# Optimization experiments

Hardware: AMD Instinct MI355X
Metric: run time of the kernel (lower is better)

## Reference

```python
import jax, jax.numpy as jnp
import numpy as np
from jax import lax

N, D, H, E = 8192, 1024, 4096, 8


def setup_inputs() -> dict:
    key = jax.random.key(0)
    ks = jax.random.split(key, 4)
    return {
        "x": jax.random.normal(ks[0], (N, D), dtype=jnp.float32),
        "wg": jax.random.normal(ks[1], (D, E), dtype=jnp.float32) * 0.001,
        "fc1_w": jax.random.normal(ks[2], (E, D, H), dtype=jnp.float32) * 0.001,
        "fc1_b": jnp.zeros((E, 1, H), dtype=jnp.float32),
        "fc2_w": jax.random.normal(ks[3], (E, H, D), dtype=jnp.float32) * 0.001,
        "fc2_b": jnp.zeros((E, 1, D), dtype=jnp.float32),
        "k": 2,
    }


def reference(x, wg, fc1_w, fc1_b, fc2_w, fc2_b, k):
    n, d = x.shape
    e = wg.shape[1]
    cap = (k * n) // e  # expert capacity (capacity factor 1.0)

    # --- gate ---
    scores = jax.nn.softmax(x @ wg, axis=-1)          # [N,E]
    topv, topi = lax.top_k(scores, k)                 # [N,k]

    # --- top-k routing: position of each (token, slot) within its expert buffer ---
    masks = jax.nn.one_hot(topi, e, dtype=jnp.int32)  # [N,k,E]
    # slot-major priority: all slot-0 assignments before slot-1
    m = jnp.transpose(masks, (1, 0, 2)).reshape(k * n, e)
    pos_flat = jnp.cumsum(m, axis=0) - m              # position before own assignment
    pos = jnp.sum(pos_flat * m, axis=1).reshape(k, n).T   # [N,k]
    valid = pos < cap                                  # capacity overflow -> dropped

    # --- load-balance aux loss (top-1 fraction * mean gate prob) ---
    me = scores.mean(axis=0)                           # [E]
    ce = masks[:, 0, :].astype(scores.dtype).mean(axis=0)
    l_aux = e * jnp.sum(me * ce)

    # --- encode (dispatch): scatter tokens into [E, C, D] buffers ---
    w = valid.astype(x.dtype)                          # [N,k]
    flat_idx = topi * cap + jnp.where(valid, pos, 0)   # [N,k]
    contrib = (x[:, None, :] * w[:, :, None]).reshape(-1, d)
    dispatched = jnp.zeros((e * cap, d), x.dtype).at[flat_idx.reshape(-1)].add(contrib)
    dispatched = dispatched.reshape(e, cap, d)

    # --- batched expert FFN (all-to-all is identity on one device) ---
    h = jax.nn.relu(jnp.einsum('ecd,edh->ech', dispatched, fc1_w) + fc1_b)
    y = jnp.einsum('ech,ehd->ecd', h, fc2_w) + fc2_b   # [E,C,D]

    # --- decode (combine): gather back and weight by gate scores ---
    gathered = y.reshape(e * cap, d)[flat_idx]         # [N,k,D]
    output = jnp.einsum('nk,nkd->nd', topv * w, gathered)
    return output, l_aux
```

## Files before the change

### kernel.cpp

```cpp
#include <hip/hip_runtime.h>
#include <hip/hip_bf16.h>
#include <stdint.h>

#define N_TOK 8192
#define DMODEL 1024
#define HDIM 4096
#define NEXP 8
#define CAP 2048
#define GATE_BLOCKS (N_TOK / 4)

typedef float floatx4 __attribute__((ext_vector_type(4)));
typedef int int32x4_t __attribute__((ext_vector_type(4)));
typedef int int32x8_t __attribute__((ext_vector_type(8)));

static __device__ __forceinline__ void async_copy16(const void* g, void* l) {
  __builtin_amdgcn_global_load_lds(
      (const __attribute__((address_space(1))) void*)g,
      (__attribute__((address_space(3))) void*)l, 16, 0, 0);
}

static __device__ __forceinline__ unsigned int pk4_fp8(float a, float b, float c, float d) {
  int r = __builtin_amdgcn_cvt_pk_fp8_f32(a, b, 0, 0);
  r = __builtin_amdgcn_cvt_pk_fp8_f32(c, d, r, 1);
  return (unsigned int)r;
}

static __device__ __forceinline__ unsigned short f2bf(float f) {
  union { float f; uint32_t u; } v; v.f = f;
  uint32_t r = (v.u + 0x7FFFu + ((v.u >> 16) & 1u)) >> 16;
  return (unsigned short)r;
}

static __device__ __forceinline__ float bf2f(unsigned short u) {
  union { float f; uint32_t u32; } v; v.u32 = ((uint32_t)u) << 16;
  return v.f;
}

__global__ __launch_bounds__(256) void gate_kernel(
    const float* __restrict__ x, const float* __restrict__ wg,
    float* __restrict__ topv, int* __restrict__ topi,
    float* __restrict__ me_part, int* __restrict__ ce_part) {
  __shared__ float sm_p[4][NEXP];
  __shared__ int sm_i0[4];
  int wave = threadIdx.x >> 6;
  int lane = threadIdx.x & 63;
  int n = blockIdx.x * 4 + wave;
  float acc[NEXP];
#pragma unroll
  for (int e = 0; e < NEXP; e++) acc[e] = 0.f;
  const float* xr = x + (size_t)n * DMODEL;
#pragma unroll 4
  for (int i = 0; i < DMODEL / 64; i++) {
    int idx = lane + 64 * i;
    float xv = xr[idx];
    const float4* wr = (const float4*)(wg + (size_t)idx * NEXP);
    float4 w0 = wr[0], w1 = wr[1];
    acc[0] += xv * w0.x; acc[1] += xv * w0.y;
    acc[2] += xv * w0.z; acc[3] += xv * w0.w;
    acc[4] += xv * w1.x; acc[5] += xv * w1.y;
    acc[6] += xv * w1.z; acc[7] += xv * w1.w;
  }
#pragma unroll
  for (int e = 0; e < NEXP; e++) {
    float v = acc[e];
#pragma unroll
    for (int off = 32; off > 0; off >>= 1) v += __shfl_down(v, off, 64);
    acc[e] = v;
  }
  if (lane == 0) {
    float mx = acc[0];
#pragma unroll
    for (int e = 1; e < NEXP; e++) mx = fmaxf(mx, acc[e]);
    float p[NEXP]; float s = 0.f;
#pragma unroll
    for (int e = 0; e < NEXP; e++) { p[e] = expf(acc[e] - mx); s += p[e]; }
    float inv = 1.f / s;
#pragma unroll
    for (int e = 0; e < NEXP; e++) p[e] *= inv;
    int i0 = 0; float v0 = p[0];
#pragma unroll
    for (int e = 1; e < NEXP; e++) if (p[e] > v0) { v0 = p[e]; i0 = e; }
    int i1 = -1; float v1 = -1.f;
#pragma unroll
    for (int e = 0; e < NEXP; e++) {
      if (e == i0) continue;
      if (p[e] > v1) { v1 = p[e]; i1 = e; }
    }
    topv[n * 2] = v0; topv[n * 2 + 1] = v1;
    topi[n * 2] = i0; topi[n * 2 + 1] = i1;
#pragma unroll
    for (int e = 0; e < NEXP; e++) sm_p[wave][e] = p[e];
    sm_i0[wave] = i0;
  }
  __syncthreads();
  if (threadIdx.x < NEXP) {
    int e = threadIdx.x;
    float pm = 0.f; int cc = 0;
#pragma unroll
    for (int w = 0; w < 4; w++) {
      pm += sm_p[w][e];
      cc += (sm_i0[w] == e) ? 1 : 0;
    }
    me_part[blockIdx.x * NEXP + e] = pm;
    ce_part[blockIdx.x * NEXP + e] = cc;
  }
}

__global__ __launch_bounds__(1024) void scan_kernel(
    const int* __restrict__ topi, const float* __restrict__ topv,
    int* __restrict__ flat_idx, float* __restrict__ cw) {
  __shared__ int hist[16][NEXP];
  __shared__ int base[NEXP];
  int tid = threadIdx.x;
  int w = tid >> 6, lane = tid & 63;
  if (tid < NEXP) base[tid] = 0;
  int vals[16];
#pragma unroll
  for (int c = 0; c < 16; c++) {
    int j = c * 1024 + tid;
    vals[c] = topi[(size_t)(j & 8191) * 2 + (j >> 13)];
  }
  __syncthreads();
  for (int c = 0; c < 16; c++) {
    int j = c * 1024 + tid;
    int slot = j >> 13;
    int n = j & 8191;
    int e = vals[c];
    int rank = 0;
#pragma unroll
    for (int ee = 0; ee < NEXP; ee++) {
      unsigned long long m = __ballot(e == ee);
      if (e == ee) rank = __popcll(m & ((1ull << lane) - 1ull));
      if (lane == ee) hist[w][ee] = __popcll(m);
    }
    __syncthreads();
    if (tid < NEXP) {
      int run = base[tid];
#pragma unroll
      for (int ww = 0; ww < 16; ww++) {
        int t = hist[ww][tid];
        hist[ww][tid] = run;
        run += t;
      }
      base[tid] = run;
    }
    __syncthreads();
    int pos = hist[w][e] + rank;
    bool valid = pos < CAP;
    flat_idx[n * 2 + slot] = e * CAP + (valid ? pos : 0);
    cw[n * 2 + slot] = valid ? topv[n * 2 + slot] : 0.f;
    __syncthreads();
  }
}

__global__ __launch_bounds__(256) void transpose_cvt_fp8(
    const float* __restrict__ in, unsigned char* __restrict__ out,
    int R, int C) {
  __shared__ float tile[32][129];
  const float* inp = in + (size_t)blockIdx.z * R * C;
  unsigned char* outp = out + (size_t)blockIdx.z * R * C;
  int c0 = blockIdx.x * 32, r0 = blockIdx.y * 128;
  int t = threadIdx.x;
#pragma unroll
  for (int p = 0; p < 4; p++) {
    int r = p * 32 + (t >> 3);
    int c4 = (t & 7) * 4;
    float4 v = *(const float4*)(inp + (size_t)(r0 + r) * C + c0 + c4);
    tile[c4 + 0][r] = v.x; tile[c4 + 1][r] = v.y;
    tile[c4 + 2][r] = v.z; tile[c4 + 3][r] = v.w;
  }
  __syncthreads();
  int c = t >> 3, r16 = (t & 7) * 16;
  unsigned int w[4];
#pragma unroll
  for (int j = 0; j < 4; j++) {
    float a = tile[c][r16 + j * 4 + 0] * 512.f;
    float b = tile[c][r16 + j * 4 + 1] * 512.f;
    float cc2 = tile[c][r16 + j * 4 + 2] * 512.f;
    float d = tile[c][r16 + j * 4 + 3] * 512.f;
    w[j] = pk4_fp8(a, b, cc2, d);
  }
  uint4 o; o.x = w[0]; o.y = w[1]; o.z = w[2]; o.w = w[3];
  *(uint4*)(outp + (size_t)(c0 + c) * R + r0 + r16) = o;
}

__global__ __launch_bounds__(64) void dispatch_kernel(
    const float* __restrict__ x, const int* __restrict__ flat_idx,
    const float* __restrict__ cw, unsigned char* __restrict__ disp) {
  int a = blockIdx.x;
  if (cw[a] == 0.f) return;
  int n = a >> 1;
  int f = flat_idx[a];
  int lane = threadIdx.x;
  const float4* xr = (const float4*)(x + (size_t)n * DMODEL);
  unsigned int* dr = (unsigned int*)(disp + (size_t)f * DMODEL);
#pragma unroll
  for (int i = 0; i < 4; i++) {
    float4 v = xr[lane + 64 * i];
    dr[lane + 64 * i] = pk4_fp8(v.x, v.y, v.z, v.w);
  }
}

template <int K_DIM, bool RELU, int OUT_MODE>
__global__ __launch_bounds__(512) void gemm_fp8_kernel(
    const unsigned char* __restrict__ A, const unsigned char* __restrict__ BT,
    const float* __restrict__ bias, void* __restrict__ Cout, int M, int Ncols,
    float inv_scale, float out_mult) {
  constexpr int BK = 128;
  constexpr int NSTAGE = K_DIM / BK;
  static_assert(NSTAGE >= 2, "need >=2 K stages for the 2-deep pipeline");
  __shared__ unsigned char As[2][256 * BK];
  __shared__ unsigned char Bs[2][256 * BK];

  int e = blockIdx.z, tm = blockIdx.y, tn = blockIdx.x;
  const unsigned char* Ae = A + (size_t)e * M * K_DIM + (size_t)tm * 256 * K_DIM;
  const unsigned char* Be = BT + (size_t)e * Ncols * K_DIM + (size_t)tn * 256 * K_DIM;
  int wv = threadIdx.x >> 6, l = threadIdx.x & 63;
  int wm = wv >> 2, wn = wv & 3;
  int l15 = l & 15, quad = l >> 4;
  int rbase = wv * 8 + (l >> 3);
  int cg = (l & 7) ^ ((l >> 3) & 7);
  floatx4 acc[8][4] = {};

#define STAGE_LOADS(k0, buf)                                                   \
  {                                                                            \
    _Pragma("unroll") for (int i = 0; i < 4; i++) {                            \
      int r = rbase + i * 64;                                                  \
      async_copy16(Ae + (size_t)r * K_DIM + (k0) + cg * 16,                    \
                   &As[buf][i * 8192 + wv * 1024]);                            \
      async_copy16(Be + (size_t)r * K_DIM + (k0) + cg * 16,                    \
                   &Bs[buf][i * 8192 + wv * 1024]);                            \
    }                                                                          \
  }

#define READ_BF(ni)                                                            \
  {                                                                            \
    int m = wn * 64 + (ni) * 16 + l15;                                         \
    int x0 = (quad * 2) ^ (m & 7), x1 = (quad * 2 + 1) ^ (m & 7);              \
    int32x4_t lo = *(const int32x4_t*)(&Bs[cur][m * 128 + x0 * 16]);           \
    int32x4_t hi = *(const int32x4_t*)(&Bs[cur][m * 128 + x1 * 16]);           \
    bf[ni] = __builtin_shufflevector(lo, hi, 0, 1, 2, 3, 4, 5, 6, 7);          \
  }

#define READ_AF(dst, mi)                                                       \
  {                                                                            \
    int m = wm * 128 + (mi) * 16 + l15;                                        \
    int x0 = (quad * 2) ^ (m & 7), x1 = (quad * 2 + 1) ^ (m & 7);              \
    int32x4_t lo = *(const int32x4_t*)(&As[cur][m * 128 + x0 * 16]);           \
    int32x4_t hi = *(const int32x4_t*)(&As[cur][m * 128 + x1 * 16]);           \
    (dst) = __builtin_shufflevector(lo, hi, 0, 1, 2, 3, 4, 5, 6, 7);           \
  }

#define MFMA_ROW(asrc, mi)                                                     \
  _Pragma("unroll") for (int ni = 0; ni < 4; ni++)                             \
      acc[mi][ni] = __builtin_amdgcn_mfma_scale_f32_16x16x128_f8f6f4(          \
          (asrc), bf[ni], acc[mi][ni], 0, 0, 0, 0x7F7F7F7F, 0, 0x7F7F7F7F);

  STAGE_LOADS(0, 0);
  STAGE_LOADS(BK, 1);
#pragma unroll
  for (int s = 0; s < NSTAGE; s++) {
    const int cur = s & 1;
    if (s + 1 < NSTAGE)
      asm volatile("s_waitcnt vmcnt(8)" ::: "memory");
    else
      asm volatile("s_waitcnt vmcnt(0)" ::: "memory");
    __builtin_amdgcn_s_barrier();
    int32x8_t afA[4], afB[4], bf[4];
    READ_BF(0); READ_BF(1); READ_BF(2); READ_BF(3);
    READ_AF(afA[0], 0);
    __builtin_amdgcn_sched_barrier(0);
    READ_AF(afA[1], 1);
    __builtin_amdgcn_sched_barrier(0);
    READ_AF(afA[2], 2);
    __builtin_amdgcn_sched_barrier(0);
    READ_AF(afA[3], 3);
    __builtin_amdgcn_sched_barrier(0);
    __builtin_amdgcn_s_setprio(1);
    asm volatile("s_waitcnt lgkmcnt(6)" ::: "memory");
    __builtin_amdgcn_sched_barrier(0);
    MFMA_ROW(afA[0], 0);
    asm volatile("s_waitcnt lgkmcnt(4)" ::: "memory");
    __builtin_amdgcn_sched_barrier(0);
    MFMA_ROW(afA[1], 1);
    asm volatile("s_waitcnt lgkmcnt(2)" ::: "memory");
    __builtin_amdgcn_sched_barrier(0);
    MFMA_ROW(afA[2], 2);
    asm volatile("s_waitcnt lgkmcnt(0)" ::: "memory");
    __builtin_amdgcn_sched_barrier(0);
    MFMA_ROW(afA[3], 3);
    __builtin_amdgcn_s_setprio(0);
    READ_AF(afB[0], 4);
    __builtin_amdgcn_sched_barrier(0);
    READ_AF(afB[1], 5);
    __builtin_amdgcn_sched_barrier(0);
    READ_AF(afB[2], 6);
    __builtin_amdgcn_sched_barrier(0);
    READ_AF(afB[3], 7);
    __builtin_amdgcn_sched_barrier(0);
    __builtin_amdgcn_s_setprio(1);
    asm volatile("s_waitcnt lgkmcnt(6)" ::: "memory");
    __builtin_amdgcn_sched_barrier(0);
    MFMA_ROW(afB[0], 4);
    asm volatile("s_waitcnt lgkmcnt(4)" ::: "memory");
    __builtin_amdgcn_sched_barrier(0);
    MFMA_ROW(afB[1], 5);
    asm volatile("s_waitcnt lgkmcnt(2)" ::: "memory");
    __builtin_amdgcn_sched_barrier(0);
    MFMA_ROW(afB[2], 6);
    asm volatile("s_waitcnt lgkmcnt(0)" ::: "memory");
    __builtin_amdgcn_sched_barrier(0);
    __builtin_amdgcn_s_setprio(0);
    __builtin_amdgcn_s_barrier();
    if (s + 2 < NSTAGE) STAGE_LOADS((s + 2) * BK, cur);
    __builtin_amdgcn_s_setprio(1);
    MFMA_ROW(afB[3], 7);
    __builtin_amdgcn_s_setprio(0);
  }
#undef STAGE_LOADS
#undef READ_BF
#undef READ_AF
#undef MFMA_ROW

  int row_base = tm * 256 + wm * 128;
  int col_base = tn * 256 + wn * 64;
  const float* be = bias + (size_t)e * Ncols;
#pragma unroll
  for (int ni = 0; ni < 4; ni++) {
    int col = col_base + ni * 16 + l15;
    float bv = be[col];
#pragma unroll
    for (int mi = 0; mi < 8; mi++) {
#pragma unroll
      for (int r = 0; r < 4; r++) {
        int row = row_base + mi * 16 + quad * 4 + r;
        float v = acc[mi][ni][r] * inv_scale + bv;
        if (RELU) v = fmaxf(v, 0.f);
        size_t idx = (size_t)e * M * Ncols + (size_t)row * Ncols + col;
        if (OUT_MODE == 1) {
          float s = fminf(fmaxf(v * out_mult, -440.f), 440.f);
          unsigned int b8 = (unsigned int)__builtin_amdgcn_cvt_pk_fp8_f32(s, s, 0, 0) & 0xFF;
          ((unsigned char*)Cout)[idx] = (unsigned char)b8;
        } else if (OUT_MODE == 2) {
          ((unsigned short*)Cout)[idx] = f2bf(v);
        } else {
          ((float*)Cout)[idx] = v;
        }
      }
    }
  }
}

__global__ __launch_bounds__(256) void combine_kernel(
    const unsigned short* __restrict__ y, const int* __restrict__ flat_idx,
    const float* __restrict__ cw, float* __restrict__ out) {
  int n = blockIdx.x;
  float w0 = cw[n * 2], w1 = cw[n * 2 + 1];
  int f0 = flat_idx[n * 2], f1 = flat_idx[n * 2 + 1];
  const ushort2* y0 = (const ushort2*)(y + (size_t)f0 * DMODEL);
  const ushort2* y1 = (const ushort2*)(y + (size_t)f1 * DMODEL);
  float2* o = (float2*)(out + (size_t)n * DMODEL);
  int t = threadIdx.x;
#pragma unroll
  for (int i = 0; i < 2; i++) {
    int j = t + i * 256;
    ushort2 a = y0[j], b = y1[j];
    float2 r;
    r.x = w0 * bf2f(a.x) + w1 * bf2f(b.x);
    r.y = w0 * bf2f(a.y) + w1 * bf2f(b.y);
    o[j] = r;
  }
}

__global__ __launch_bounds__(256) void laux_kernel(
    const float* __restrict__ me_part, const int* __restrict__ ce_part,
    float* __restrict__ out_laux) {
  __shared__ float sme[NEXP][33];
  __shared__ float sce[NEXP][33];
  int tid = threadIdx.x;
  int e = tid >> 5;
  int c = tid & 31;
  float pm = 0.f, cc = 0.f;
  for (int b = c; b < GATE_BLOCKS; b += 32) {
    pm += me_part[b * NEXP + e];
    cc += (float)ce_part[b * NEXP + e];
  }
  sme[e][c] = pm;
  sce[e][c] = cc;
  __syncthreads();
  if (tid < NEXP) {
    float tm = 0.f, tc = 0.f;
#pragma unroll
    for (int i = 0; i < 32; i++) { tm += sme[tid][i]; tc += sce[tid][i]; }
    sme[tid][32] = tm;
    sce[tid][32] = tc;
  }
  __syncthreads();
  if (tid == 0) {
    float s = 0.f;
#pragma unroll
    for (int ee = 0; ee < NEXP; ee++)
      s += (sme[ee][32] / (float)N_TOK) * (sce[ee][32] / (float)N_TOK);
    *out_laux = (float)NEXP * s;
  }
}

extern "C" void kernel_launch(void* const* d_in, const int* in_sizes, int n_in,
                              void* d_out, int out_size, void* d_ws,
                              size_t ws_size, hipStream_t stream) {
  (void)in_sizes; (void)n_in; (void)out_size; (void)ws_size;
  const float* x     = (const float*)d_in[0];
  const float* wg    = (const float*)d_in[1];
  const float* fc1_w = (const float*)d_in[2];
  const float* fc1_b = (const float*)d_in[3];
  const float* fc2_w = (const float*)d_in[4];
  const float* fc2_b = (const float*)d_in[5];
  float* out = (float*)d_out;

  char* ws = (char*)d_ws;
  size_t o = 0;
  unsigned char* fc1t = (unsigned char*)(ws + o); o += (size_t)NEXP * DMODEL * HDIM;
  unsigned char* fc2t = (unsigned char*)(ws + o); o += (size_t)NEXP * DMODEL * HDIM;
  unsigned char* disp = (unsigned char*)(ws + o); o += (size_t)NEXP * CAP * DMODEL;
  unsigned char* hbuf = (unsigned char*)(ws + o); o += (size_t)NEXP * CAP * HDIM;
  unsigned short* ybuf = (unsigned short*)(ws + o); o += (size_t)NEXP * CAP * DMODEL * 2;
  float* topv = (float*)(ws + o); o += (size_t)N_TOK * 2 * 4;
  int* topi   = (int*)(ws + o);   o += (size_t)N_TOK * 2 * 4;
  int* flat   = (int*)(ws + o);   o += (size_t)N_TOK * 2 * 4;
  float* cw   = (float*)(ws + o); o += (size_t)N_TOK * 2 * 4;
  float* mep  = (float*)(ws + o); o += (size_t)GATE_BLOCKS * NEXP * 4;
  int* cep    = (int*)(ws + o);   o += (size_t)GATE_BLOCKS * NEXP * 4;


  gate_kernel<<<GATE_BLOCKS, 256, 0, stream>>>(x, wg, topv, topi, mep, cep);
  scan_kernel<<<1, 1024, 0, stream>>>(topi, topv, flat, cw);
  transpose_cvt_fp8<<<dim3(HDIM / 32, DMODEL / 128, NEXP), 256, 0, stream>>>(fc1_w, fc1t, DMODEL, HDIM);
  transpose_cvt_fp8<<<dim3(DMODEL / 32, HDIM / 128, NEXP), 256, 0, stream>>>(fc2_w, fc2t, HDIM, DMODEL);
  dispatch_kernel<<<N_TOK * 2, 64, 0, stream>>>(x, flat, cw, disp);
  gemm_fp8_kernel<DMODEL, true, 1>
      <<<dim3(HDIM / 256, CAP / 256, NEXP), 512, 0, stream>>>(
          disp, fc1t, fc1_b, hbuf, CAP, HDIM, 1.f / 512.f, 16.f);
  gemm_fp8_kernel<HDIM, false, 2>
      <<<dim3(DMODEL / 256, CAP / 256, NEXP), 512, 0, stream>>>(
          hbuf, fc2t, fc2_b, ybuf, CAP, DMODEL, 1.f / 8192.f, 1.f);
  combine_kernel<<<N_TOK, 256, 0, stream>>>(ybuf, flat, cw, out);
  laux_kernel<<<1, 256, 0, stream>>>(mep, cep, out + (size_t)N_TOK * DMODEL);
}
```

Before: 581.7 us.

## Restructure FP8 GEMM main loop into four-phase ping-pong schedule with interleaved prefetch

Replaces the two-stage-ahead prefetch loop with a one-stage-ahead schedule split into four phases per K step. Each phase reads two A fragments, optionally issues part of the next stage's global-to-LDS loads, then runs two MFMA rows between barriers. The goal is to spread memory traffic across the compute phases and cut register pressure by holding only two A fragments at a time. In exchange it adds more barriers per iteration, waits on vmcnt(0) with only one stage in flight, and disables loop unrolling, all of which can expose load latency.

```diff
diff --git a/kernel.cpp b/kernel.cpp
--- a/kernel.cpp
+++ b/kernel.cpp
@@ -222,15 +222,13 @@
   int cg = (l & 7) ^ ((l >> 3) & 7);
   floatx4 acc[8][4] = {};
 
-#define STAGE_LOADS(k0, buf)                                                   \
+#define GLOAD(i, buf, k0)                                                      \
   {                                                                            \
-    _Pragma("unroll") for (int i = 0; i < 4; i++) {                            \
-      int r = rbase + i * 64;                                                  \
-      async_copy16(Ae + (size_t)r * K_DIM + (k0) + cg * 16,                    \
-                   &As[buf][i * 8192 + wv * 1024]);                            \
-      async_copy16(Be + (size_t)r * K_DIM + (k0) + cg * 16,                    \
-                   &Bs[buf][i * 8192 + wv * 1024]);                            \
-    }                                                                          \
+    int r = rbase + (i) * 64;                                                  \
+    async_copy16(Ae + (size_t)r * K_DIM + (k0) + cg * 16,                      \
+                 &As[buf][(i) * 8192 + wv * 1024]);                            \
+    async_copy16(Be + (size_t)r * K_DIM + (k0) + cg * 16,                      \
+                 &Bs[buf][(i) * 8192 + wv * 1024]);                            \
   }
 
 #define READ_BF(ni)                                                            \
@@ -256,71 +254,43 @@
       acc[mi][ni] = __builtin_amdgcn_mfma_scale_f32_16x16x128_f8f6f4(          \
           (asrc), bf[ni], acc[mi][ni], 0, 0, 0, 0x7F7F7F7F, 0, 0x7F7F7F7F);
 
-  STAGE_LOADS(0, 0);
-  STAGE_LOADS(BK, 1);
-#pragma unroll
+#define PHASE_TAIL(r0, r1)                                                     \
+  __builtin_amdgcn_s_barrier();                                                \
+  asm volatile("s_waitcnt lgkmcnt(0)" ::: "memory");                           \
+  __builtin_amdgcn_sched_barrier(0);                                           \
+  __builtin_amdgcn_s_setprio(1);                                               \
+  MFMA_ROW(a0, r0);                                                            \
+  MFMA_ROW(a1, r1);                                                            \
+  __builtin_amdgcn_s_setprio(0);                                               \
+  __builtin_amdgcn_sched_barrier(0);                                           \
+  __builtin_amdgcn_s_barrier();
+
+  GLOAD(0, 0, 0); GLOAD(1, 0, 0); GLOAD(2, 0, 0); GLOAD(3, 0, 0);
+#pragma unroll 1
   for (int s = 0; s < NSTAGE; s++) {
-    const int cur = s & 1;
-    if (s + 1 < NSTAGE)
-      asm volatile("s_waitcnt vmcnt(8)" ::: "memory");
-    else
-      asm volatile("s_waitcnt vmcnt(0)" ::: "memory");
+    const int cur = s & 1, nxt = cur ^ 1;
+    const int knext = (s + 1) * BK;
+    const bool pf = (s + 1 < NSTAGE);
+    asm volatile("s_waitcnt vmcnt(0)" ::: "memory");
     __builtin_amdgcn_s_barrier();
-    int32x8_t afA[4], afB[4], bf[4];
+    int32x8_t bf[4], a0, a1;
     READ_BF(0); READ_BF(1); READ_BF(2); READ_BF(3);
-    READ_AF(afA[0], 0);
-    __builtin_amdgcn_sched_barrier(0);
-    READ_AF(afA[1], 1);
-    __builtin_amdgcn_sched_barrier(0);
-    READ_AF(afA[2], 2);
-    __builtin_amdgcn_sched_barrier(0);
-    READ_AF(afA[3], 3);
-    __builtin_amdgcn_sched_barrier(0);
-    __builtin_amdgcn_s_setprio(1);
-    asm volatile("s_waitcnt lgkmcnt(6)" ::: "memory");
-    __builtin_amdgcn_sched_barrier(0);
-    MFMA_ROW(afA[0], 0);
-    asm volatile("s_waitcnt lgkmcnt(4)" ::: "memory");
-    __builtin_amdgcn_sched_barrier(0);
-    MFMA_ROW(afA[1], 1);
-    asm volatile("s_waitcnt lgkmcnt(2)" ::: "memory");
-    __builtin_amdgcn_sched_barrier(0);
-    MFMA_ROW(afA[2], 2);
-    asm volatile("s_waitcnt lgkmcnt(0)" ::: "memory");
-    __builtin_amdgcn_sched_barrier(0);
-    MFMA_ROW(afA[3], 3);
-    __builtin_amdgcn_s_setprio(0);
-    READ_AF(afB[0], 4);
-    __builtin_amdgcn_sched_barrier(0);
-    READ_AF(afB[1], 5);
-    __builtin_amdgcn_sched_barrier(0);
-    READ_AF(afB[2], 6);
-    __builtin_amdgcn_sched_barrier(0);
-    READ_AF(afB[3], 7);
-    __builtin_amdgcn_sched_barrier(0);
-    __builtin_amdgcn_s_setprio(1);
-    asm volatile("s_waitcnt lgkmcnt(6)" ::: "memory");
-    __builtin_amdgcn_sched_barrier(0);
-    MFMA_ROW(afB[0], 4);
-    asm volatile("s_waitcnt lgkmcnt(4)" ::: "memory");
-    __builtin_amdgcn_sched_barrier(0);
-    MFMA_ROW(afB[1], 5);
-    asm volatile("s_waitcnt lgkmcnt(2)" ::: "memory");
-    __builtin_amdgcn_sched_barrier(0);
-    MFMA_ROW(afB[2], 6);
-    asm volatile("s_waitcnt lgkmcnt(0)" ::: "memory");
-    __builtin_amdgcn_sched_barrier(0);
-    __builtin_amdgcn_s_setprio(0);
-    __builtin_amdgcn_s_barrier();
-    if (s + 2 < NSTAGE) STAGE_LOADS((s + 2) * BK, cur);
-    __builtin_amdgcn_s_setprio(1);
-    MFMA_ROW(afB[3], 7);
-    __builtin_amdgcn_s_setprio(0);
-  }
-#undef STAGE_LOADS
+    READ_AF(a0, 0); READ_AF(a1, 1);
+    if (pf) { GLOAD(0, nxt, knext); GLOAD(1, nxt, knext); }
+    PHASE_TAIL(0, 1);
+    READ_AF(a0, 2); READ_AF(a1, 3);
+    if (pf) { GLOAD(2, nxt, knext); GLOAD(3, nxt, knext); }
+    PHASE_TAIL(2, 3);
+    READ_AF(a0, 4); READ_AF(a1, 5);
+    PHASE_TAIL(4, 5);
+    READ_AF(a0, 6); READ_AF(a1, 7);
+    PHASE_TAIL(6, 7);
+  }
+#undef GLOAD
 #undef READ_BF
 #undef READ_AF
 #undef MFMA_ROW
+#undef PHASE_TAIL
 
   int row_base = tm * 256 + wm * 128;
   int col_base = tn * 256 + wn * 64;
```

Result: slower. 603.1 us (+3.7%).
